# Kernel optimization log

Measured on AMD Instinct MI355X. Metric: run time of the kernel, lower is better.

Reference implementation:

```python
import jax, jax.numpy as jnp
import numpy as np

AMP = 2  # from init_kwargs

def setup_inputs() -> dict:
    key = jax.random.key(0)
    k1, k2 = jax.random.split(key)
    B, C, H, W = 4, 32, 256, 256
    x_q = jax.random.normal(k1, (B, C, H, W), dtype=jnp.float32)
    x_k = jax.random.normal(k2, (B, C, H, W), dtype=jnp.float32)
    return {"x_q": x_q, "x_k": x_k, "num_heads": 4}


def reference(x_q, x_k, num_heads):
    amp = AMP
    ks = 2 * amp + 1  # kernel_size
    B, C, H, W = x_q.shape
    head_dim = C // num_heads
    scale = head_dim ** (-0.5)
    # (B, head_dim, heads, H, W)
    q = x_q.reshape(B, head_dim, num_heads, H, W) * scale
    k = x_k.reshape(B, head_dim, num_heads, H, W)
    k_pad = jnp.pad(k, ((0, 0), (0, 0), (0, 0), (amp, amp), (amp, amp)))
    # validity mask: padded region is invalid (mask < 0.5 in original)
    valid = jnp.pad(jnp.ones((H, W), dtype=x_q.dtype), ((amp, amp), (amp, amp)))
    attn = []
    for i in range(ks):  # static loop over 25 offsets
        for j in range(ks):
            # per-offset dot product over head_dim -> (B, heads, H, W)
            a = jnp.sum(q * k_pad[:, :, :, i:i + H, j:j + W], axis=1)
            a = jnp.where(valid[i:i + H, j:j + W] > 0.5, a, jnp.asarray(-1000.0, a.dtype))
            attn.append(a)
    attn = jnp.stack(attn, axis=1)          # (B, ks*ks, heads, H, W)
    attn = jax.nn.softmax(attn, axis=1)
    # offset grid: arange(-s//2+1, s//2+1) == [-amp, ..., amp]
    offs = jnp.arange(-amp, amp + 1, dtype=x_q.dtype)
    grid = jnp.stack(jnp.meshgrid(offs, offs, indexing='ij'), axis=-1).reshape(ks * ks, 2)
    # offset-weighted sum over the ks*ks window positions -> (B, 2, heads, H, W)
    v_ = jnp.einsum('bkhxy,kc->bchxy', attn, grid)
    # mean over heads -> (B, 2, H, W)
    return jnp.mean(v_, axis=2)
```

## Files before the change

kernel.cpp:

```cpp
#include <hip/hip_runtime.h>

#define Bdim 4
#define Cdim 32
#define NH   4
#define HD   8
#define Hdim 256
#define Wdim 256
#define AMP  2
#define KS   5

#define XT    32
#define TY    8
#define TROWS 12
#define TPOS  44
#define NPAIRS 16
#define PAIR_STRIDE (TROWS * TPOS)
#define TILE_SLOTS (NPAIRS * PAIR_STRIDE)

typedef _Float16 h2 __attribute__((ext_vector_type(2)));

static __device__ __forceinline__ float dot2acc(h2 a, h2 b, float c) {
#if __has_builtin(__builtin_amdgcn_fdot2)
    return __builtin_amdgcn_fdot2(a, b, c, false);
#else
    return c + (float)a.x * (float)b.x + (float)a.y * (float)b.y;
#endif
}

__global__ __launch_bounds__(256) void natt_offset_kernel(
    const float* __restrict__ xq,
    const float* __restrict__ xk,
    float* __restrict__ out)
{
    __shared__ __align__(16) float kt[TILE_SLOTS];

    const int tid = threadIdx.x;
    const int bid = blockIdx.x;
    const int r8  = bid & 7;
    const int u   = bid >> 3;
    const int yt  = r8 * 4 + (u & 3);
    const int rst = u >> 2;
    const int xt  = rst & 7;
    const int b   = rst >> 3;

    const int Y0 = yt * TY;
    const int X0 = xt * XT;

    const int h    = tid >> 6;
    const int lane = tid & 63;
    const int row  = lane >> 3;
    const int qx   = lane & 7;
    const int y    = Y0 + row;
    const int x0   = X0 + qx * 4;

    const size_t plane = (size_t)Hdim * Wdim;
    const float scale = 0.35355339059327373f;

    {
        const float* kb = xk + (size_t)b * Cdim * plane;
        #pragma unroll
        for (int it = 0; it < 8; ++it) {
            const int j = tid + it * 256;
            if (j < NPAIRS * TROWS * 10) {
                const int c4 = j % 10;
                const int t  = j / 10;
                const int rw = t % TROWS;
                const int p2 = t / TROWS;
                const int hh = p2 & 3;
                const int d0 = (p2 >> 2) * 2;
                const int c0 = d0 * NH + hh;
                int yr = Y0 - AMP + rw;
                yr = yr < 0 ? 0 : (yr > Hdim - 1 ? Hdim - 1 : yr);
                const int xs = X0 - 6 + c4 * 4;
                const int xc = xs < 0 ? 0 : (xs > Wdim - 4 ? Wdim - 4 : xs);
                const int sh = xs - xc;
                const float* pa = kb + (size_t)c0 * plane + (size_t)yr * Wdim + xc;
                const float4 va = *(const float4*)pa;
                const float4 vb = *(const float4*)(pa + 4 * plane);
                const float a[4]  = {va.x, va.y, va.z, va.w};
                const float bb[4] = {vb.x, vb.y, vb.z, vb.w};
                float o[4];
                #pragma unroll
                for (int k2 = 0; k2 < 4; ++k2) {
                    int idx = k2 + sh;
                    idx = idx < 0 ? 0 : (idx > 3 ? 3 : idx);
                    h2 pk;
                    pk.x = (_Float16)a[idx];
                    pk.y = (_Float16)bb[idx];
                    o[k2] = __builtin_bit_cast(float, pk);
                }
                *(float4*)(kt + p2 * PAIR_STRIDE + rw * TPOS + c4 * 4) =
                    make_float4(o[0], o[1], o[2], o[3]);
            }
        }
    }

    const float* qb = xq + (size_t)b * Cdim * plane + (size_t)y * Wdim + x0;
    h2 q2[4][4];
    #pragma unroll
    for (int d2 = 0; d2 < 4; ++d2) {
        const float4 qa = *(const float4*)(qb + (size_t)((2 * d2)     * NH + h) * plane);
        const float4 qc = *(const float4*)(qb + (size_t)((2 * d2 + 1) * NH + h) * plane);
        const float qa4[4] = {qa.x, qa.y, qa.z, qa.w};
        const float qc4[4] = {qc.x, qc.y, qc.z, qc.w};
        #pragma unroll
        for (int p = 0; p < 4; ++p) {
            q2[d2][p].x = (_Float16)(qa4[p] * scale);
            q2[d2][p].y = (_Float16)(qc4[p] * scale);
        }
    }

    __syncthreads();

    float Z[4]  = {0.f, 0.f, 0.f, 0.f};
    float sx[4] = {0.f, 0.f, 0.f, 0.f};
    float sy[4] = {0.f, 0.f, 0.f, 0.f};

    #pragma unroll
    for (int r = 0; r < KS; ++r) {
        float dot[KS][4];
        #pragma unroll
        for (int dj = 0; dj < KS; ++dj) {
            dot[dj][0] = 0.f; dot[dj][1] = 0.f; dot[dj][2] = 0.f; dot[dj][3] = 0.f;
        }

        #pragma unroll
        for (int d2 = 0; d2 < 4; ++d2) {
            const float* wp = kt + ((d2 << 2) | h) * PAIR_STRIDE
                                 + (row + r) * TPOS + (qx * 4 + 4);
            const float4 wa = *(const float4*)wp;
            const float4 wb = *(const float4*)(wp + 4);
            const float wf[8] = {wa.x, wa.y, wa.z, wa.w, wb.x, wb.y, wb.z, wb.w};
            h2 w[8];
            #pragma unroll
            for (int k2 = 0; k2 < 8; ++k2) w[k2] = __builtin_bit_cast(h2, wf[k2]);
            #pragma unroll
            for (int dj = 0; dj < KS; ++dj) {
                #pragma unroll
                for (int p = 0; p < 4; ++p)
                    dot[dj][p] = dot2acc(q2[d2][p], w[p + dj], dot[dj][p]);
            }
        }

        const int yy = y + r - AMP;
        const bool rowok = (yy >= 0) && (yy < Hdim);
        const float fdi = (float)(r - AMP);
        #pragma unroll
        for (int p = 0; p < 4; ++p) {
            float e[KS];
            #pragma unroll
            for (int dj = 0; dj < KS; ++dj) {
                const int xx = x0 + p + dj - AMP;
                const bool ok = rowok && (xx >= 0) && (xx < Wdim);
                e[dj] = ok ? __expf(dot[dj][p]) : 0.f;
            }
            const float er = ((e[0] + e[1]) + (e[2] + e[3])) + e[4];
            Z[p]  += er;
            sx[p] += fdi * er;
            sy[p] += (e[3] - e[1]) + 2.f * (e[4] - e[0]);
        }
    }

    __syncthreads();
    float* red = kt;
    const int pxl = row * XT + qx * 4;
    {
        const float i0 = 1.f / Z[0], i1 = 1.f / Z[1], i2 = 1.f / Z[2], i3 = 1.f / Z[3];
        *(float4*)(red + (h * 2 + 0) * (XT * TY) + pxl) =
            make_float4(sx[0]*i0, sx[1]*i1, sx[2]*i2, sx[3]*i3);
        *(float4*)(red + (h * 2 + 1) * (XT * TY) + pxl) =
            make_float4(sy[0]*i0, sy[1]*i1, sy[2]*i2, sy[3]*i3);
    }
    __syncthreads();

    if (h < 2) {
        float acc[4] = {0.f, 0.f, 0.f, 0.f};
        #pragma unroll
        for (int hh = 0; hh < NH; ++hh) {
            const float4 v = *(const float4*)(red + (hh * 2 + h) * (XT * TY) + pxl);
            acc[0] += v.x; acc[1] += v.y; acc[2] += v.z; acc[3] += v.w;
        }
        *(float4*)(out + ((size_t)b * 2 + h) * plane + (size_t)y * Wdim + x0) =
            make_float4(acc[0]*0.25f, acc[1]*0.25f, acc[2]*0.25f, acc[3]*0.25f);
    }
}

extern "C" void kernel_launch(void* const* d_in, const int* in_sizes, int n_in,
                              void* d_out, int out_size, void* d_ws, size_t ws_size,
                              hipStream_t stream) {
    const float* xq = (const float*)d_in[0];
    const float* xk = (const float*)d_in[1];
    float* out = (float*)d_out;

    natt_offset_kernel<<<dim3(1024, 1, 1), dim3(256, 1, 1), 0, stream>>>(xq, xk, out);
}
```

Measured before the change: 105.6 us.

## Split heads into separate single-wave blocks with partial buffer and mean kernel

```diff
diff --git a/kernel.cpp b/kernel.cpp
--- a/kernel.cpp
+++ b/kernel.cpp
@@ -13,7 +13,7 @@
 #define TY    8
 #define TROWS 12
 #define TPOS  44
-#define NPAIRS 16
+#define NPAIRS 4
 #define PAIR_STRIDE (TROWS * TPOS)
 #define TILE_SLOTS (NPAIRS * PAIR_STRIDE)
 
@@ -27,31 +27,32 @@
 #endif
 }
 
-__global__ __launch_bounds__(256) void natt_offset_kernel(
+__global__ __launch_bounds__(64, 4) void natt_head_kernel(
     const float* __restrict__ xq,
     const float* __restrict__ xk,
-    float* __restrict__ out)
+    float* __restrict__ part)
 {
     __shared__ __align__(16) float kt[TILE_SLOTS];
 
-    const int tid = threadIdx.x;
-    const int bid = blockIdx.x;
-    const int r8  = bid & 7;
+    const int lane = threadIdx.x;
+    const int bid  = blockIdx.x;
+    const int xcd = bid & 7;
     const int u   = bid >> 3;
-    const int yt  = r8 * 4 + (u & 3);
-    const int rst = u >> 2;
-    const int xt  = rst & 7;
-    const int b   = rst >> 3;
+    const int yt  = xcd * 4 + (u & 3);
+    const int v   = u >> 2;
+    const int xt  = v & 7;
+    const int w2  = v >> 3;
+    const int h   = w2 & 3;
+    const int b   = w2 >> 2;
 
     const int Y0 = yt * TY;
     const int X0 = xt * XT;
-
-    const int h    = tid >> 6;
-    const int lane = tid & 63;
-    const int row  = lane >> 3;
-    const int qx   = lane & 7;
-    const int y    = Y0 + row;
-    const int x0   = X0 + qx * 4;
+    const bool interior = (yt != 0) && (yt != 31) && (xt != 0) && (xt != 7);
+
+    const int row = lane >> 3;
+    const int qx  = lane & 7;
+    const int y   = Y0 + row;
+    const int x0  = X0 + qx * 4;
 
     const size_t plane = (size_t)Hdim * Wdim;
     const float scale = 0.35355339059327373f;
@@ -60,15 +61,13 @@
         const float* kb = xk + (size_t)b * Cdim * plane;
         #pragma unroll
         for (int it = 0; it < 8; ++it) {
-            const int j = tid + it * 256;
+            const int j = lane + it * 64;
             if (j < NPAIRS * TROWS * 10) {
                 const int c4 = j % 10;
                 const int t  = j / 10;
                 const int rw = t % TROWS;
                 const int p2 = t / TROWS;
-                const int hh = p2 & 3;
-                const int d0 = (p2 >> 2) * 2;
-                const int c0 = d0 * NH + hh;
+                const int c0 = (2 * p2) * NH + h;
                 int yr = Y0 - AMP + rw;
                 yr = yr < 0 ? 0 : (yr > Hdim - 1 ? Hdim - 1 : yr);
                 const int xs = X0 - 6 + c4 * 4;
@@ -126,8 +125,7 @@
 
         #pragma unroll
         for (int d2 = 0; d2 < 4; ++d2) {
-            const float* wp = kt + ((d2 << 2) | h) * PAIR_STRIDE
-                                 + (row + r) * TPOS + (qx * 4 + 4);
+            const float* wp = kt + d2 * PAIR_STRIDE + (row + r) * TPOS + (qx * 4 + 4);
             const float4 wa = *(const float4*)wp;
             const float4 wb = *(const float4*)(wp + 4);
             const float wf[8] = {wa.x, wa.y, wa.z, wa.w, wb.x, wb.y, wb.z, wb.w};
@@ -142,47 +140,62 @@
             }
         }
 
-        const int yy = y + r - AMP;
-        const bool rowok = (yy >= 0) && (yy < Hdim);
         const float fdi = (float)(r - AMP);
-        #pragma unroll
-        for (int p = 0; p < 4; ++p) {
-            float e[KS];
-            #pragma unroll
-            for (int dj = 0; dj < KS; ++dj) {
-                const int xx = x0 + p + dj - AMP;
-                const bool ok = rowok && (xx >= 0) && (xx < Wdim);
-                e[dj] = ok ? __expf(dot[dj][p]) : 0.f;
-            }
-            const float er = ((e[0] + e[1]) + (e[2] + e[3])) + e[4];
-            Z[p]  += er;
-            sx[p] += fdi * er;
-            sy[p] += (e[3] - e[1]) + 2.f * (e[4] - e[0]);
+        if (interior) {
+            #pragma unroll
+            for (int p = 0; p < 4; ++p) {
+                float e[KS];
+                #pragma unroll
+                for (int dj = 0; dj < KS; ++dj) e[dj] = __expf(dot[dj][p]);
+                const float er = ((e[0] + e[1]) + (e[2] + e[3])) + e[4];
+                Z[p]  += er;
+                sx[p] += fdi * er;
+                sy[p] += (e[3] - e[1]) + 2.f * (e[4] - e[0]);
+            }
+        } else {
+            const int yy = y + r - AMP;
+            const bool rowok = (yy >= 0) && (yy < Hdim);
+            #pragma unroll
+            for (int p = 0; p < 4; ++p) {
+                float e[KS];
+                #pragma unroll
+                for (int dj = 0; dj < KS; ++dj) {
+                    const int xx = x0 + p + dj - AMP;
+                    const bool ok = rowok && (xx >= 0) && (xx < Wdim);
+                    e[dj] = ok ? __expf(dot[dj][p]) : 0.f;
+                }
+                const float er = ((e[0] + e[1]) + (e[2] + e[3])) + e[4];
+                Z[p]  += er;
+                sx[p] += fdi * er;
+                sy[p] += (e[3] - e[1]) + 2.f * (e[4] - e[0]);
+            }
         }
     }
 
-    __syncthreads();
-    float* red = kt;
-    const int pxl = row * XT + qx * 4;
-    {
-        const float i0 = 1.f / Z[0], i1 = 1.f / Z[1], i2 = 1.f / Z[2], i3 = 1.f / Z[3];
-        *(float4*)(red + (h * 2 + 0) * (XT * TY) + pxl) =
-            make_float4(sx[0]*i0, sx[1]*i1, sx[2]*i2, sx[3]*i3);
-        *(float4*)(red + (h * 2 + 1) * (XT * TY) + pxl) =
-            make_float4(sy[0]*i0, sy[1]*i1, sy[2]*i2, sy[3]*i3);
-    }
-    __syncthreads();
-
-    if (h < 2) {
-        float acc[4] = {0.f, 0.f, 0.f, 0.f};
-        #pragma unroll
-        for (int hh = 0; hh < NH; ++hh) {
-            const float4 v = *(const float4*)(red + (hh * 2 + h) * (XT * TY) + pxl);
-            acc[0] += v.x; acc[1] += v.y; acc[2] += v.z; acc[3] += v.w;
-        }
-        *(float4*)(out + ((size_t)b * 2 + h) * plane + (size_t)y * Wdim + x0) =
-            make_float4(acc[0]*0.25f, acc[1]*0.25f, acc[2]*0.25f, acc[3]*0.25f);
-    }
+    const float i0 = 1.f / Z[0], i1 = 1.f / Z[1], i2 = 1.f / Z[2], i3 = 1.f / Z[3];
+    const size_t pbase = (size_t)((h * Bdim + b) * 2) * plane + (size_t)y * Wdim + x0;
+    *(float4*)(part + pbase)         = make_float4(sx[0]*i0, sx[1]*i1, sx[2]*i2, sx[3]*i3);
+    *(float4*)(part + pbase + plane) = make_float4(sy[0]*i0, sy[1]*i1, sy[2]*i2, sy[3]*i3);
+}
+
+__global__ __launch_bounds__(256) void head_mean_kernel(
+    const float* __restrict__ part,
+    float* __restrict__ out)
+{
+    const int idx = blockIdx.x * 256 + threadIdx.x;
+    const int pq  = (int)(((size_t)Hdim * Wdim) / 4);
+    const int g   = idx / pq;
+    const int r   = idx % pq;
+    const float4* p4 = (const float4*)part;
+    float4 a = p4[(0 * 8 + g) * pq + r];
+    const float4 b1 = p4[(1 * 8 + g) * pq + r];
+    const float4 b2 = p4[(2 * 8 + g) * pq + r];
+    const float4 b3 = p4[(3 * 8 + g) * pq + r];
+    a.x = (a.x + b1.x + b2.x + b3.x) * 0.25f;
+    a.y = (a.y + b1.y + b2.y + b3.y) * 0.25f;
+    a.z = (a.z + b1.z + b2.z + b3.z) * 0.25f;
+    a.w = (a.w + b1.w + b2.w + b3.w) * 0.25f;
+    ((float4*)out)[idx] = a;
 }
 
 extern "C" void kernel_launch(void* const* d_in, const int* in_sizes, int n_in,
@@ -190,7 +203,9 @@
                               hipStream_t stream) {
     const float* xq = (const float*)d_in[0];
     const float* xk = (const float*)d_in[1];
-    float* out = (float*)d_out;
-
-    natt_offset_kernel<<<dim3(1024, 1, 1), dim3(256, 1, 1), 0, stream>>>(xq, xk, out);
-}
+    float* out  = (float*)d_out;
+    float* part = (float*)d_ws;
+
+    natt_head_kernel<<<dim3(4096, 1, 1), dim3(64, 1, 1), 0, stream>>>(xq, xk, part);
+    head_mean_kernel<<<dim3(512, 1, 1), dim3(256, 1, 1), 0, stream>>>(part, out);
+}
```

New measurement: 104.8 us. About the same (-0.7%).
